# Kernel optimization log

Measured on AMD Instinct MI355X. Metric: run time of the kernel, lower is better.

Reference implementation:

```python
import jax, jax.numpy as jnp
import numpy as np

B, N, E = 128, 400, 512      # batch, spatial locations, encoder_size
SH, H, A = 256, 512, 256     # structural_hidden, cell_content_hidden, attention_size
EMB, V, T = 256, 1000, 256   # embedding_size, vocabulary_size, num_timesteps
START = 0                    # token2integer['<start>']


def setup_inputs() -> dict:
    key = jax.random.key(0)
    ks = jax.random.split(key, 16)
    s = lambda k, shape, scale=0.05: jax.random.normal(k, shape, jnp.float32) * scale
    return {
        'encoded_features_map': jax.random.normal(ks[0], (B, N, E), jnp.float32),
        'structural_hidden_state': jax.random.normal(ks[1], (1, B, SH), jnp.float32),
        'cell_content_target': jax.random.randint(ks[2], (B, T), 0, V),
        # attention params (linear projections + score vector)
        'Wf': s(ks[3], (E, A)), 'bf': jnp.zeros((A,), jnp.float32),
        'Ws': s(ks[4], (SH, A)), 'bs': jnp.zeros((A,), jnp.float32),
        'Wc': s(ks[5], (H, A)), 'bc': jnp.zeros((A,), jnp.float32),
        'v_att': s(ks[6], (A,)),
        # embedding table
        'emb_table': s(ks[7], (V, EMB), 0.02),
        # GRU params (torch layout: [3H, in] / [3H, H], gate order r,z,n)
        'W_ih': s(ks[8], (3 * H, E + EMB)), 'W_hh': s(ks[9], (3 * H, H)),
        'b_ih': jnp.zeros((3 * H,), jnp.float32), 'b_hh': jnp.zeros((3 * H,), jnp.float32),
        # output projection
        'W_fc': s(ks[10], (H, V)), 'b_fc': jnp.zeros((V,), jnp.float32),
    }


def _decode(encoded_features_map, structural_hidden_state, cell_content_target,
            Wf, bf, Ws, bs, Wc, bc, v_att, emb_table, W_ih, W_hh, b_ih, b_hh, W_fc, b_fc):
    # precompute static attention projections
    feat_proj = jnp.einsum('bne,ea->bna', encoded_features_map, Wf) + bf   # [B,N,A]
    struct_proj = structural_hidden_state[0] @ Ws + bs                      # [B,A]

    def step(carry, tok_next):
        h, tok = carry                                  # h: [B,H], tok: [B]
        # additive attention over spatial locations
        att = jnp.tanh(feat_proj + (struct_proj + h @ Wc + bc)[:, None, :])  # [B,N,A]
        alpha = jax.nn.softmax(att @ v_att, axis=-1)                          # [B,N]
        context = jnp.einsum('bn,bne->be', alpha, encoded_features_map)      # [B,E]
        # embed previous token, concat, single GRU step
        x = jnp.concatenate([context, emb_table[tok]], axis=1)               # [B,E+EMB]
        gi = x @ W_ih.T + b_ih                                               # [B,3H]
        gh = h @ W_hh.T + b_hh                                               # [B,3H]
        r = jax.nn.sigmoid(gi[:, :H] + gh[:, :H])
        z = jax.nn.sigmoid(gi[:, H:2 * H] + gh[:, H:2 * H])
        n = jnp.tanh(gi[:, 2 * H:] + r * gh[:, 2 * H:])
        h_new = (1.0 - z) * n + z * h
        logits = h_new @ W_fc + b_fc                                         # [B,V]
        # per-step CrossEntropyLoss (mean over batch), teacher forcing
        logp = jax.nn.log_softmax(logits, axis=-1)
        loss_t = -jnp.mean(jnp.take_along_axis(logp, tok_next[:, None], axis=1))
        return (h_new, tok_next), (logits, loss_t)

    h0 = jnp.zeros((encoded_features_map.shape[0], H), jnp.float32)
    tok0 = jnp.full((encoded_features_map.shape[0],), START, cell_content_target.dtype)
    tgt_t = cell_content_target.T                                            # [T,B]
    _, (predictions, losses) = jax.lax.scan(step, (h0, tok0), tgt_t)
    nT = tgt_t.shape[0]
    bsz = encoded_features_map.shape[0]
    loss = losses.sum() / nT / bsz
    return predictions, loss


def reference(encoded_features_map, structural_hidden_state, cell_content_target,
              Wf, bf, Ws, bs, Wc, bc, v_att, emb_table, W_ih, W_hh, b_ih, b_hh, W_fc, b_fc):
    return _decode(encoded_features_map, structural_hidden_state, cell_content_target,
                   Wf, bf, Ws, bs, Wc, bc, v_att, emb_table, W_ih, W_hh, b_ih, b_hh, W_fc, b_fc)
```

## Files before the change

kernel.cpp:

```cpp
#include <hip/hip_runtime.h>
#include <math.h>

#define BB  128
#define NN  400
#define EE  512
#define SHD 256
#define HH  512
#define AA  256
#define EMBD 256
#define VV  1000
#define TT  256
#define TH3 (3*HH)
#define BNROWS (BB*NN)
#define PRED_STRIDE (BB*VV)
#define NPRED ((size_t)TT*BB*VV)

__device__ __forceinline__ float tanh_fast(float x){
    float e = __expf(2.f*x);
    return 1.f - 2.f*__builtin_amdgcn_rcpf(e + 1.f);
}


__global__ void k_zero(float* __restrict__ hbuf0, float* __restrict__ loss_acc){
    int i = blockIdx.x*blockDim.x + threadIdx.x;
    if (i < BB*HH) hbuf0[i] = 0.f;
    if (i == 0) loss_acc[0] = 0.f;
}

__global__ __launch_bounds__(256) void k_featproj(
    const float* __restrict__ feats, const float* __restrict__ Wf,
    const float* __restrict__ bf, float* __restrict__ fp)
{
    __shared__ float As[32][65];
    __shared__ float Bs[32][65];
    int row0 = blockIdx.x*64, col0 = blockIdx.y*64;
    int tx = threadIdx.x & 15, ty = threadIdx.x >> 4;
    float acc[4][4] = {};
    for (int k0 = 0; k0 < EE; k0 += 32){
        for (int idx = threadIdx.x; idx < 64*32; idx += 256){
            int r = idx >> 5, kk = idx & 31;
            As[kk][r] = feats[(size_t)(row0 + r)*EE + k0 + kk];
        }
        for (int idx = threadIdx.x; idx < 32*64; idx += 256){
            int kk = idx >> 6, c = idx & 63;
            Bs[kk][c] = Wf[(size_t)(k0 + kk)*AA + col0 + c];
        }
        __syncthreads();
        #pragma unroll
        for (int kk = 0; kk < 32; ++kk){
            float a0 = As[kk][ty*4+0], a1 = As[kk][ty*4+1], a2 = As[kk][ty*4+2], a3 = As[kk][ty*4+3];
            float b0 = Bs[kk][tx*4+0], b1 = Bs[kk][tx*4+1], b2 = Bs[kk][tx*4+2], b3 = Bs[kk][tx*4+3];
            acc[0][0] += a0*b0; acc[0][1] += a0*b1; acc[0][2] += a0*b2; acc[0][3] += a0*b3;
            acc[1][0] += a1*b0; acc[1][1] += a1*b1; acc[1][2] += a1*b2; acc[1][3] += a1*b3;
            acc[2][0] += a2*b0; acc[2][1] += a2*b1; acc[2][2] += a2*b2; acc[2][3] += a2*b3;
            acc[3][0] += a3*b0; acc[3][1] += a3*b1; acc[3][2] += a3*b2; acc[3][3] += a3*b3;
        }
        __syncthreads();
    }
    #pragma unroll
    for (int i = 0; i < 4; ++i){
        #pragma unroll
        for (int j = 0; j < 4; ++j){
            int col = col0 + tx*4 + j;
            fp[(size_t)(row0 + ty*4 + i)*AA + col] = acc[i][j] + bf[col];
        }
    }
}

__global__ void k_wembT(const float* __restrict__ Wih, float* __restrict__ wT){
    int i = blockIdx.x*blockDim.x + threadIdx.x;
    if (i >= EMBD*TH3) return;
    int m = i / TH3, r = i - m*TH3;
    wT[i] = Wih[(size_t)r*(EE+EMBD) + EE + m];
}

__global__ __launch_bounds__(256) void k_embproj(
    const float* __restrict__ emb, const float* __restrict__ wT,
    const float* __restrict__ bih, float* __restrict__ ep)
{
    __shared__ float el[16][257];
    int vt = blockIdx.x, rc = blockIdx.y;
    for (int idx = threadIdx.x; idx < 16*EMBD; idx += 256){
        int v = idx >> 8, m = idx & 255;
        int gv = vt*16 + v;
        el[v][m] = (gv < VV) ? emb[(size_t)gv*EMBD + m] : 0.f;
    }
    __syncthreads();
    int r = rc*256 + threadIdx.x;
    float acc[16] = {};
    for (int m = 0; m < EMBD; ++m){
        float w = wT[(size_t)m*TH3 + r];
        #pragma unroll
        for (int v = 0; v < 16; ++v) acc[v] += el[v][m]*w;
    }
    float bb_ = bih[r];
    #pragma unroll
    for (int v = 0; v < 16; ++v){
        int gv = vt*16 + v;
        if (gv < VV) ep[(size_t)gv*TH3 + r] = acc[v] + bb_;
    }
}

__global__ void k_structproj(const float* __restrict__ sh, const float* __restrict__ Ws,
                             const float* __restrict__ bs, float* __restrict__ sp){
    __shared__ float sl[SHD];
    int b = blockIdx.x;
    for (int i = threadIdx.x; i < SHD; i += 256) sl[i] = sh[(size_t)b*SHD + i];
    __syncthreads();
    int a = threadIdx.x;
    float acc = 0.f;
    for (int s = 0; s < SHD; ++s) acc += sl[s]*Ws[(size_t)s*AA + a];
    sp[(size_t)b*AA + a] = acc + bs[a];
}


__device__ __forceinline__ void logits_body(int tpred, int bt, int vt,
    const float* __restrict__ hsrc, const float* __restrict__ Wfc,
    const float* __restrict__ bfc, float* __restrict__ preds, float* hl)
{
    for (int idx = threadIdx.x; idx < 8*HH; idx += 512){
        int bl = idx >> 9;
        hl[idx] = hsrc[(size_t)(bt*8+bl)*HH + (idx & 511)];
    }
    __syncthreads();
    for (int o = threadIdx.x; o < 1000; o += 512){
        int bl = o / 125, vl = o - bl*125;
        int v = vt*125 + vl;
        const float* wcol = Wfc + v;
        const float* hrow = hl + bl*HH;
        float acc = 0.f;
        #pragma unroll 4
        for (int h = 0; h < HH; ++h) acc += hrow[h]*wcol[(size_t)h*VV];
        __builtin_nontemporal_store(acc + bfc[v],
            &preds[(size_t)tpred*PRED_STRIDE + (size_t)(bt*8+bl)*VV + v]);
    }
}

__device__ __forceinline__ void loss_body(int tpred, int lb,
    const float* __restrict__ preds, const int* __restrict__ tgt, float* loss_acc)
{
    int w = threadIdx.x >> 6, lane = threadIdx.x & 63;
    float contrib = 0.f;
    for (int rr = 0; rr < 2; ++rr){
        int row = lb*16 + w*2 + rr;
        const float* p = preds + (size_t)tpred*PRED_STRIDE + (size_t)row*VV;
        float m = -1e30f;
        for (int i = lane; i < VV; i += 64) m = fmaxf(m, __builtin_nontemporal_load(p + i));
        #pragma unroll
        for (int off = 32; off; off >>= 1) m = fmaxf(m, __shfl_xor(m, off));
        float s = 0.f;
        for (int i = lane; i < VV; i += 64) s += expf(__builtin_nontemporal_load(p + i) - m);
        #pragma unroll
        for (int off = 32; off; off >>= 1) s += __shfl_xor(s, off);
        if (lane == 0) contrib += m + logf(s) - p[tgt[(size_t)row*TT + tpred]];
    }
    if (lane == 0) atomicAdd(loss_acc, contrib);
}

__global__ __launch_bounds__(512) void k_attn(int t,
    const float* __restrict__ fp, const float* __restrict__ feats,
    const float* __restrict__ sp, const float* __restrict__ bc,
    const float* __restrict__ vatt, const float* __restrict__ qpart,
    const float* __restrict__ hin, const float* __restrict__ Wfc,
    const float* __restrict__ bfc,
    float* __restrict__ pctx, float* __restrict__ psum, float* __restrict__ preds)
{
    __shared__ __align__(16) float smem[AA + 8*EE + 8];
    if (blockIdx.x >= 256){
        if (t == 0) return;
        int lb = blockIdx.x - 256;
        logits_body(t-1, lb >> 3, lb & 7, hin, Wfc, bfc, preds, smem);
        return;
    }
    int b = blockIdx.x >> 1, half = blockIdx.x & 1;
    float* qs = smem;
    float* px = smem + AA;
    float* ps = smem + AA + 8*EE;
    if (threadIdx.x < AA){
        int a = threadIdx.x;
        float val = sp[(size_t)b*AA + a] + bc[a];
        if (t > 0){
            #pragma unroll 4
            for (int jt = 0; jt < 32; ++jt) val += qpart[((size_t)jt*BB + b)*AA + a];
        }
        qs[a] = val;
    }
    __syncthreads();
    int w = threadIdx.x >> 6, lane = threadIdx.x & 63;
    float4 v4 = ((const float4*)vatt)[lane];
    float4 q4 = ((const float4*)qs)[lane];
    float acc0=0,acc1=0,acc2=0,acc3=0,acc4=0,acc5=0,acc6=0,acc7=0;
    float psum_r = 0.f;
    const int nbase = half*200;
    for (int k = 0; k < 25; ++k){
        int n = nbase + w + 8*k;
        const float4* fr4 = (const float4*)(fp + ((size_t)b*NN + n)*AA);
        float4 xv = fr4[lane];
        float s = v4.x*tanh_fast(xv.x+q4.x) + v4.y*tanh_fast(xv.y+q4.y)
                + v4.z*tanh_fast(xv.z+q4.z) + v4.w*tanh_fast(xv.w+q4.w);
        #pragma unroll
        for (int off = 32; off; off >>= 1) s += __shfl_xor(s, off);
        float e = __expf(s);
        psum_r += e;
        const float4* f4 = (const float4*)(feats + ((size_t)b*NN + n)*EE) + lane*2;
        float4 fa = f4[0], fb = f4[1];
        acc0 += e*fa.x; acc1 += e*fa.y; acc2 += e*fa.z; acc3 += e*fa.w;
        acc4 += e*fb.x; acc5 += e*fb.y; acc6 += e*fb.z; acc7 += e*fb.w;
    }
    float* myrow = px + w*EE + lane*8;
    myrow[0]=acc0; myrow[1]=acc1; myrow[2]=acc2; myrow[3]=acc3;
    myrow[4]=acc4; myrow[5]=acc5; myrow[6]=acc6; myrow[7]=acc7;
    if (lane == 0) ps[w] = psum_r;
    __syncthreads();
    for (int e = threadIdx.x; e < EE; e += 512){
        float tot = 0.f;
        #pragma unroll
        for (int ww = 0; ww < 8; ++ww) tot += px[ww*EE + e];
        pctx[((size_t)b*2 + half)*EE + e] = tot;
    }
    if (threadIdx.x == 0){
        float tot = 0.f;
        #pragma unroll
        for (int ww = 0; ww < 8; ++ww) tot += ps[ww];
        psum[b*2 + half] = tot;
    }
}

__global__ __launch_bounds__(512) void k_gru(int t,
    const float* __restrict__ pctx, const float* __restrict__ psum,
    const float* __restrict__ hin, float* __restrict__ hout,
    const float* __restrict__ Wih, const float* __restrict__ Whh,
    const float* __restrict__ bhh, const float* __restrict__ embp,
    const int* __restrict__ tgt, const float* __restrict__ Wc,
    float* __restrict__ qpart, const float* __restrict__ preds,
    float* __restrict__ loss_acc)
{
    if (blockIdx.x >= 256){
        if (t == 0) return;
        loss_body(t-1, (int)blockIdx.x - 256, preds, tgt, loss_acc);
        return;
    }
    __shared__ __align__(16) float stage[16][516];
    __shared__ float part[2][16][16][3];
    __shared__ float gi_s[16][16][3];
    __shared__ float hn_l[16][16];
    __shared__ float inv_l[16];
    int bt = blockIdx.x >> 5, jt = blockIdx.x & 31;
    int bg = bt*16, jbase = jt*16;
    int p = threadIdx.x & 255, role = threadIdx.x >> 8;
    int b = p & 15, j = p >> 4, r0 = jbase + j;
    if (threadIdx.x < 16){
        int bb_ = threadIdx.x;
        inv_l[bb_] = 1.f/(psum[(bg+bb_)*2] + psum[(bg+bb_)*2+1]);
    }
    __syncthreads();
    for (int idx = threadIdx.x; idx < 16*EE; idx += 512){
        int bb_ = idx >> 9, e = idx & 511;
        stage[bb_][e] = (pctx[((size_t)(bg+bb_)*2)*EE + e] +
                         pctx[((size_t)(bg+bb_)*2+1)*EE + e]) * inv_l[bb_];
    }
    __syncthreads();
    {
        const float* w0 = Wih + (size_t)r0*(EE+EMBD);
        const float* w1 = w0 + (size_t)512*(EE+EMBD);
        const float* w2 = w0 + (size_t)1024*(EE+EMBD);
        float ar=0, az=0, an=0;
        int e0 = role*256;
        const float4* srow = (const float4*)&stage[b][0];
        #pragma unroll 4
        for (int e4 = e0/4; e4 < e0/4 + 64; ++e4){
            float4 c = srow[e4];
            int e = e4*4;
            ar += c.x*w0[e] + c.y*w0[e+1] + c.z*w0[e+2] + c.w*w0[e+3];
            az += c.x*w1[e] + c.y*w1[e+1] + c.z*w1[e+2] + c.w*w1[e+3];
            an += c.x*w2[e] + c.y*w2[e+1] + c.z*w2[e+2] + c.w*w2[e+3];
        }
        part[role][b][j][0] = ar; part[role][b][j][1] = az; part[role][b][j][2] = an;
    }
    __syncthreads();
    if (threadIdx.x < 256){
        int tok = (t == 0) ? 0 : tgt[(size_t)(bg+b)*TT + (t-1)];
        const float* er = embp + (size_t)tok*TH3 + r0;
        gi_s[b][j][0] = part[0][b][j][0] + part[1][b][j][0] + er[0];
        gi_s[b][j][1] = part[0][b][j][1] + part[1][b][j][1] + er[512];
        gi_s[b][j][2] = part[0][b][j][2] + part[1][b][j][2] + er[1024];
    }
    __syncthreads();
    for (int idx = threadIdx.x; idx < 16*HH; idx += 512){
        int bb_ = idx >> 9, e = idx & 511;
        stage[bb_][e] = hin[(size_t)(bg+bb_)*HH + e];
    }
    __syncthreads();
    {
        const float* w0 = Whh + (size_t)r0*HH;
        const float* w1 = w0 + (size_t)512*HH;
        const float* w2 = w0 + (size_t)1024*HH;
        float ar=0, az=0, an=0;
        int e0 = role*256;
        const float4* srow = (const float4*)&stage[b][0];
        #pragma unroll 4
        for (int e4 = e0/4; e4 < e0/4 + 64; ++e4){
            float4 c = srow[e4];
            int e = e4*4;
            ar += c.x*w0[e] + c.y*w0[e+1] + c.z*w0[e+2] + c.w*w0[e+3];
            az += c.x*w1[e] + c.y*w1[e+1] + c.z*w1[e+2] + c.w*w1[e+3];
            an += c.x*w2[e] + c.y*w2[e+1] + c.z*w2[e+2] + c.w*w2[e+3];
        }
        part[role][b][j][0] = ar; part[role][b][j][1] = az; part[role][b][j][2] = an;
    }
    __syncthreads();
    if (threadIdx.x < 256){
        float ghr = part[0][b][j][0] + part[1][b][j][0] + bhh[r0];
        float ghz = part[0][b][j][1] + part[1][b][j][1] + bhh[r0+512];
        float ghn = part[0][b][j][2] + part[1][b][j][2] + bhh[r0+1024];
        float rr = 1.f/(1.f + expf(-(gi_s[b][j][0] + ghr)));
        float zz = 1.f/(1.f + expf(-(gi_s[b][j][1] + ghz)));
        float nn = tanhf(gi_s[b][j][2] + rr*ghn);
        float hval = stage[b][r0];
        float hn = (1.f - zz)*nn + zz*hval;
        hout[(size_t)(bg+b)*HH + r0] = hn;
        hn_l[b][j] = hn;
    }
    __syncthreads();
    for (int o = threadIdx.x; o < 16*AA; o += 512){
        int bb_ = o >> 8, a = o & 255;
        float acc = 0.f;
        #pragma unroll
        for (int jj = 0; jj < 16; ++jj) acc += hn_l[bb_][jj]*Wc[(size_t)(jbase+jj)*AA + a];
        qpart[((size_t)jt*BB + bg + bb_)*AA + a] = acc;
    }
}

__global__ __launch_bounds__(512) void k_logits_ep(int tpred, const float* __restrict__ hsrc,
    const float* __restrict__ Wfc, const float* __restrict__ bfc, float* __restrict__ preds)
{
    __shared__ __align__(16) float hl[8*HH];
    logits_body(tpred, (int)blockIdx.x >> 3, (int)blockIdx.x & 7, hsrc, Wfc, bfc, preds, hl);
}

__global__ __launch_bounds__(512) void k_loss_ep(int tpred, const float* __restrict__ preds,
    const int* __restrict__ tgt, float* __restrict__ loss_acc)
{
    loss_body(tpred, (int)blockIdx.x, preds, tgt, loss_acc);
}

__global__ void k_final(const float* __restrict__ loss_acc, float* __restrict__ out){
    out[0] = loss_acc[0] * (1.f/4194304.f);
}

extern "C" void kernel_launch(void* const* d_in, const int* in_sizes, int n_in,
                              void* d_out, int out_size, void* d_ws, size_t ws_size,
                              hipStream_t stream)
{
    const float* feats = (const float*)d_in[0];
    const float* shs   = (const float*)d_in[1];
    const int*   tgt   = (const int*)d_in[2];
    const float* Wf    = (const float*)d_in[3];
    const float* bf    = (const float*)d_in[4];
    const float* Ws    = (const float*)d_in[5];
    const float* bs    = (const float*)d_in[6];
    const float* Wc    = (const float*)d_in[7];
    const float* bc    = (const float*)d_in[8];
    const float* vatt  = (const float*)d_in[9];
    const float* emb   = (const float*)d_in[10];
    const float* Wih   = (const float*)d_in[11];
    const float* Whh   = (const float*)d_in[12];
    const float* bih   = (const float*)d_in[13];
    const float* bhh   = (const float*)d_in[14];
    const float* Wfc   = (const float*)d_in[15];
    const float* bfc   = (const float*)d_in[16];
    float* preds = (float*)d_out;

    char* base = (char*)d_ws;
    size_t off = 0;
    auto alloc = [&](size_t nfloats) -> float* {
        float* ptr = (float*)(base + off);
        off += ((nfloats*sizeof(float) + 255)/256)*256;
        return ptr;
    };
    float* fp    = alloc((size_t)BNROWS*AA);
    float* embp  = alloc((size_t)VV*TH3);
    float* wT    = alloc((size_t)EMBD*TH3);
    float* sp    = alloc((size_t)BB*AA);
    float* qpart = alloc((size_t)32*BB*AA);
    float* pctx  = alloc((size_t)BB*2*EE);
    float* psum  = alloc((size_t)BB*2);
    float* hbuf  = alloc((size_t)2*BB*HH);
    float* lacc  = alloc(16);
    (void)ws_size; (void)in_sizes; (void)n_in; (void)out_size;

    k_zero<<<(BB*HH + 511)/512, 512, 0, stream>>>(hbuf, lacc);
    k_featproj<<<dim3(BNROWS/64, AA/64), 256, 0, stream>>>(feats, Wf, bf, fp);
    k_wembT<<<(EMBD*TH3)/256, 256, 0, stream>>>(Wih, wT);
    k_embproj<<<dim3(63, TH3/256), 256, 0, stream>>>(emb, wT, bih, embp);
    k_structproj<<<BB, 256, 0, stream>>>(shs, Ws, bs, sp);

    for (int t = 0; t < TT; ++t){
        const float* hin = hbuf + (size_t)(t & 1)*BB*HH;
        float*       hout = hbuf + (size_t)((t + 1) & 1)*BB*HH;
        k_attn<<<384, 512, 0, stream>>>(t, fp, feats, sp, bc, vatt, qpart,
                                        hin, Wfc, bfc, pctx, psum, preds);
        k_gru<<<264, 512, 0, stream>>>(t, pctx, psum, hin, hout, Wih, Whh, bhh,
                                       embp, tgt, Wc, qpart, preds, lacc);
    }
    k_logits_ep<<<128, 512, 0, stream>>>(TT-1, hbuf, Wfc, bfc, preds);
    k_loss_ep<<<8, 512, 0, stream>>>(TT-1, preds, tgt, lacc);
    k_final<<<1, 1, 0, stream>>>(lacc, preds + NPRED);
}
```

Baseline: 30.90 ms.

## Transpose feature projection and FC weights, split attention into quarters, merge GRU matvecs

The feature projection is stored transposed ([B,A,N]) so attention threads each own one spatial position and read coalesced along N, and the work per batch is split across four blocks instead of two. The output FC weights are pre-transposed so the logits loop reads each vocabulary row contiguously with float4 loads. The GRU input and hidden matvecs are merged into a single pass with both operands staged in shared memory, which removes extra barriers, and the bc bias is folded into the struct projection. The trade-offs are more workspace memory, an extra transpose kernel at setup, and more partial sums to combine in the GRU stage.

New measurement: 32.84 ms. 1.06x slower.

```diff
diff --git a/kernel.cpp b/kernel.cpp
--- a/kernel.cpp
+++ b/kernel.cpp
@@ -29,7 +29,7 @@
 
 __global__ __launch_bounds__(256) void k_featproj(
     const float* __restrict__ feats, const float* __restrict__ Wf,
-    const float* __restrict__ bf, float* __restrict__ fp)
+    const float* __restrict__ bf, float* __restrict__ fpT)
 {
     __shared__ float As[32][65];
     __shared__ float Bs[32][65];
@@ -59,10 +59,12 @@
     }
     #pragma unroll
     for (int i = 0; i < 4; ++i){
+        int row = row0 + ty*4 + i;
+        int b = row/NN, n = row - b*NN;
         #pragma unroll
         for (int j = 0; j < 4; ++j){
             int col = col0 + tx*4 + j;
-            fp[(size_t)(row0 + ty*4 + i)*AA + col] = acc[i][j] + bf[col];
+            fpT[((size_t)b*AA + col)*NN + n] = acc[i][j] + bf[col];
         }
     }
 }
@@ -72,6 +74,13 @@
     if (i >= EMBD*TH3) return;
     int m = i / TH3, r = i - m*TH3;
     wT[i] = Wih[(size_t)r*(EE+EMBD) + EE + m];
+}
+
+__global__ void k_wfcT(const float* __restrict__ Wfc, float* __restrict__ WfcT){
+    int i = blockIdx.x*blockDim.x + threadIdx.x;
+    if (i >= VV*HH) return;
+    int v = i / HH, h = i - v*HH;
+    WfcT[i] = Wfc[(size_t)h*VV + v];
 }
 
 __global__ __launch_bounds__(256) void k_embproj(
@@ -102,7 +111,8 @@
 }
 
 __global__ void k_structproj(const float* __restrict__ sh, const float* __restrict__ Ws,
-                             const float* __restrict__ bs, float* __restrict__ sp){
+                             const float* __restrict__ bs, const float* __restrict__ bc,
+                             float* __restrict__ sp){
     __shared__ float sl[SHD];
     int b = blockIdx.x;
     for (int i = threadIdx.x; i < SHD; i += 256) sl[i] = sh[(size_t)b*SHD + i];
@@ -110,12 +120,12 @@
     int a = threadIdx.x;
     float acc = 0.f;
     for (int s = 0; s < SHD; ++s) acc += sl[s]*Ws[(size_t)s*AA + a];
-    sp[(size_t)b*AA + a] = acc + bs[a];
+    sp[(size_t)b*AA + a] = acc + bs[a] + bc[a];
 }
 
 
 __device__ __forceinline__ void logits_body(int tpred, int bt, int vt,
-    const float* __restrict__ hsrc, const float* __restrict__ Wfc,
+    const float* __restrict__ hsrc, const float* __restrict__ WfcT,
     const float* __restrict__ bfc, float* __restrict__ preds, float* hl)
 {
     for (int idx = threadIdx.x; idx < 8*HH; idx += 512){
@@ -126,11 +136,14 @@
     for (int o = threadIdx.x; o < 1000; o += 512){
         int bl = o / 125, vl = o - bl*125;
         int v = vt*125 + vl;
-        const float* wcol = Wfc + v;
-        const float* hrow = hl + bl*HH;
+        const float4* wrow = (const float4*)(WfcT + (size_t)v*HH);
+        const float4* hrow = (const float4*)(hl + bl*HH);
         float acc = 0.f;
-        #pragma unroll 4
-        for (int h = 0; h < HH; ++h) acc += hrow[h]*wcol[(size_t)h*VV];
+        #pragma unroll 8
+        for (int h4 = 0; h4 < HH/4; ++h4){
+            float4 w = wrow[h4], hh = hrow[h4];
+            acc += w.x*hh.x + w.y*hh.y + w.z*hh.z + w.w*hh.w;
+        }
         __builtin_nontemporal_store(acc + bfc[v],
             &preds[(size_t)tpred*PRED_STRIDE + (size_t)(bt*8+bl)*VV + v]);
     }
@@ -140,9 +153,10 @@
     const float* __restrict__ preds, const int* __restrict__ tgt, float* loss_acc)
 {
     int w = threadIdx.x >> 6, lane = threadIdx.x & 63;
+    int nw = blockDim.x >> 6;
     float contrib = 0.f;
-    for (int rr = 0; rr < 2; ++rr){
-        int row = lb*16 + w*2 + rr;
+    for (int ri = w; ri < 16; ri += nw){
+        int row = lb*16 + ri;
         const float* p = preds + (size_t)tpred*PRED_STRIDE + (size_t)row*VV;
         float m = -1e30f;
         for (int i = lane; i < VV; i += 64) m = fmaxf(m, __builtin_nontemporal_load(p + i));
@@ -158,71 +172,71 @@
 }
 
 __global__ __launch_bounds__(512) void k_attn(int t,
-    const float* __restrict__ fp, const float* __restrict__ feats,
-    const float* __restrict__ sp, const float* __restrict__ bc,
-    const float* __restrict__ vatt, const float* __restrict__ qpart,
-    const float* __restrict__ hin, const float* __restrict__ Wfc,
-    const float* __restrict__ bfc,
+    const float* __restrict__ fpT, const float* __restrict__ feats,
+    const float* __restrict__ sp2, const float* __restrict__ vatt,
+    const float* __restrict__ qpart, const float* __restrict__ hin,
+    const float* __restrict__ WfcT, const float* __restrict__ bfc,
     float* __restrict__ pctx, float* __restrict__ psum, float* __restrict__ preds)
 {
-    __shared__ __align__(16) float smem[AA + 8*EE + 8];
-    if (blockIdx.x >= 256){
+    __shared__ __align__(16) float smem[4160];
+    if (blockIdx.x >= 512){
         if (t == 0) return;
-        int lb = blockIdx.x - 256;
-        logits_body(t-1, lb >> 3, lb & 7, hin, Wfc, bfc, preds, smem);
+        int lb = blockIdx.x - 512;
+        logits_body(t-1, lb >> 3, lb & 7, hin, WfcT, bfc, preds, smem);
         return;
     }
-    int b = blockIdx.x >> 1, half = blockIdx.x & 1;
+    int b = blockIdx.x >> 2, qtr = blockIdx.x & 3;
+    const int nbase = qtr*100;
     float* qs = smem;
-    float* px = smem + AA;
-    float* ps = smem + AA + 8*EE;
+    float* vs = smem + 256;
+    float* sA = smem + 512;
+    float* al = smem + 1024;
     if (threadIdx.x < AA){
         int a = threadIdx.x;
-        float val = sp[(size_t)b*AA + a] + bc[a];
+        float val = sp2[(size_t)b*AA + a];
         if (t > 0){
             #pragma unroll 4
             for (int jt = 0; jt < 32; ++jt) val += qpart[((size_t)jt*BB + b)*AA + a];
         }
         qs[a] = val;
-    }
-    __syncthreads();
-    int w = threadIdx.x >> 6, lane = threadIdx.x & 63;
-    float4 v4 = ((const float4*)vatt)[lane];
-    float4 q4 = ((const float4*)qs)[lane];
-    float acc0=0,acc1=0,acc2=0,acc3=0,acc4=0,acc5=0,acc6=0,acc7=0;
-    float psum_r = 0.f;
-    const int nbase = half*200;
-    for (int k = 0; k < 25; ++k){
-        int n = nbase + w + 8*k;
-        const float4* fr4 = (const float4*)(fp + ((size_t)b*NN + n)*AA);
-        float4 xv = fr4[lane];
-        float s = v4.x*tanh_fast(xv.x+q4.x) + v4.y*tanh_fast(xv.y+q4.y)
-                + v4.z*tanh_fast(xv.z+q4.z) + v4.w*tanh_fast(xv.w+q4.w);
-        #pragma unroll
-        for (int off = 32; off; off >>= 1) s += __shfl_xor(s, off);
-        float e = __expf(s);
-        psum_r += e;
-        const float4* f4 = (const float4*)(feats + ((size_t)b*NN + n)*EE) + lane*2;
-        float4 fa = f4[0], fb = f4[1];
-        acc0 += e*fa.x; acc1 += e*fa.y; acc2 += e*fa.z; acc3 += e*fa.w;
-        acc4 += e*fb.x; acc5 += e*fb.y; acc6 += e*fb.z; acc7 += e*fb.w;
-    }
-    float* myrow = px + w*EE + lane*8;
-    myrow[0]=acc0; myrow[1]=acc1; myrow[2]=acc2; myrow[3]=acc3;
-    myrow[4]=acc4; myrow[5]=acc5; myrow[6]=acc6; myrow[7]=acc7;
-    if (lane == 0) ps[w] = psum_r;
-    __syncthreads();
-    for (int e = threadIdx.x; e < EE; e += 512){
-        float tot = 0.f;
-        #pragma unroll
-        for (int ww = 0; ww < 8; ++ww) tot += px[ww*EE + e];
-        pctx[((size_t)b*2 + half)*EE + e] = tot;
-    }
-    if (threadIdx.x == 0){
-        float tot = 0.f;
-        #pragma unroll
-        for (int ww = 0; ww < 8; ++ww) tot += ps[ww];
-        psum[b*2 + half] = tot;
+        vs[a] = vatt[a];
+    }
+    __syncthreads();
+    int nl = threadIdx.x & 127, ah = threadIdx.x >> 7;
+    float sacc = 0.f;
+    if (nl < 100){
+        const float* fr = fpT + ((size_t)b*AA + ah*64)*NN + nbase + nl;
+        #pragma unroll 4
+        for (int i = 0; i < 64; ++i)
+            sacc += vs[ah*64 + i]*tanh_fast(fr[(size_t)i*NN] + qs[ah*64 + i]);
+    }
+    sA[ah*128 + nl] = sacc;
+    __syncthreads();
+    if (threadIdx.x < 128){
+        float e = 0.f;
+        if (threadIdx.x < 100)
+            e = __expf(sA[threadIdx.x] + sA[128 + threadIdx.x] +
+                       sA[256 + threadIdx.x] + sA[384 + threadIdx.x]);
+        al[threadIdx.x] = e;
+    }
+    __syncthreads();
+    if (threadIdx.x < 64){
+        float e = al[threadIdx.x] + al[threadIdx.x + 64];
+        #pragma unroll
+        for (int off = 32; off; off >>= 1) e += __shfl_xor(e, off);
+        if (threadIdx.x == 0) psum[b*4 + qtr] = e;
+    }
+    {
+        int e = threadIdx.x;
+        float c0=0.f, c1=0.f, c2=0.f, c3=0.f;
+        const float* fb = feats + ((size_t)b*NN + nbase)*EE + e;
+        for (int n = 0; n < 100; n += 4){
+            c0 += al[n+0]*fb[(size_t)(n+0)*EE];
+            c1 += al[n+1]*fb[(size_t)(n+1)*EE];
+            c2 += al[n+2]*fb[(size_t)(n+2)*EE];
+            c3 += al[n+3]*fb[(size_t)(n+3)*EE];
+        }
+        pctx[((size_t)b*4 + qtr)*EE + e] = (c0+c1)+(c2+c3);
     }
 }
 
@@ -236,88 +250,71 @@
     float* __restrict__ loss_acc)
 {
     if (blockIdx.x >= 256){
-        if (t == 0) return;
-        loss_body(t-1, (int)blockIdx.x - 256, preds, tgt, loss_acc);
+        if (t > 0) loss_body(t-1, (int)blockIdx.x - 256, preds, tgt, loss_acc);
         return;
     }
-    __shared__ __align__(16) float stage[16][516];
-    __shared__ float part[2][16][16][3];
-    __shared__ float gi_s[16][16][3];
+    __shared__ __align__(16) float stC[16][516];
+    __shared__ __align__(16) float stH[16][516];
+    __shared__ float pGI[2][16][16][3];
+    __shared__ float pGH[2][16][16][3];
     __shared__ float hn_l[16][16];
-    __shared__ float inv_l[16];
     int bt = blockIdx.x >> 5, jt = blockIdx.x & 31;
     int bg = bt*16, jbase = jt*16;
     int p = threadIdx.x & 255, role = threadIdx.x >> 8;
     int b = p & 15, j = p >> 4, r0 = jbase + j;
-    if (threadIdx.x < 16){
-        int bb_ = threadIdx.x;
-        inv_l[bb_] = 1.f/(psum[(bg+bb_)*2] + psum[(bg+bb_)*2+1]);
-    }
-    __syncthreads();
+    for (int idx = threadIdx.x; idx < 16*HH; idx += 512){
+        int bb_ = idx >> 9, e = idx & 511;
+        stH[bb_][e] = hin[(size_t)(bg+bb_)*HH + e];
+    }
     for (int idx = threadIdx.x; idx < 16*EE; idx += 512){
         int bb_ = idx >> 9, e = idx & 511;
-        stage[bb_][e] = (pctx[((size_t)(bg+bb_)*2)*EE + e] +
-                         pctx[((size_t)(bg+bb_)*2+1)*EE + e]) * inv_l[bb_];
+        const float* ps4 = psum + (size_t)(bg+bb_)*4;
+        float iv = 1.f/(ps4[0]+ps4[1]+ps4[2]+ps4[3]);
+        const float* pc = pctx + (size_t)(bg+bb_)*4*EE + e;
+        stC[bb_][e] = (pc[0] + pc[EE] + pc[2*(size_t)EE] + pc[3*(size_t)EE]) * iv;
     }
     __syncthreads();
     {
-        const float* w0 = Wih + (size_t)r0*(EE+EMBD);
-        const float* w1 = w0 + (size_t)512*(EE+EMBD);
-        const float* w2 = w0 + (size_t)1024*(EE+EMBD);
-        float ar=0, az=0, an=0;
-        int e0 = role*256;
-        const float4* srow = (const float4*)&stage[b][0];
+        const float4* w0 = (const float4*)(Wih + (size_t)r0*(EE+EMBD));
+        const float4* w1 = (const float4*)(Wih + (size_t)(r0+512)*(EE+EMBD));
+        const float4* w2 = (const float4*)(Wih + (size_t)(r0+1024)*(EE+EMBD));
+        const float4* u0 = (const float4*)(Whh + (size_t)r0*HH);
+        const float4* u1 = (const float4*)(Whh + (size_t)(r0+512)*HH);
+        const float4* u2 = (const float4*)(Whh + (size_t)(r0+1024)*HH);
+        float ar=0,az=0,an=0, br=0,bz=0,bn=0;
+        const float4* crow = (const float4*)&stC[b][0];
+        const float4* hrow = (const float4*)&stH[b][0];
+        int e40 = role*64;
         #pragma unroll 4
-        for (int e4 = e0/4; e4 < e0/4 + 64; ++e4){
-            float4 c = srow[e4];
-            int e = e4*4;
-            ar += c.x*w0[e] + c.y*w0[e+1] + c.z*w0[e+2] + c.w*w0[e+3];
-            az += c.x*w1[e] + c.y*w1[e+1] + c.z*w1[e+2] + c.w*w1[e+3];
-            an += c.x*w2[e] + c.y*w2[e+1] + c.z*w2[e+2] + c.w*w2[e+3];
-        }
-        part[role][b][j][0] = ar; part[role][b][j][1] = az; part[role][b][j][2] = an;
+        for (int e4 = e40; e4 < e40 + 64; ++e4){
+            float4 c = crow[e4]; float4 h = hrow[e4];
+            float4 a0 = w0[e4], a1 = w1[e4], a2 = w2[e4];
+            float4 b0 = u0[e4], b1 = u1[e4], b2 = u2[e4];
+            ar += c.x*a0.x + c.y*a0.y + c.z*a0.z + c.w*a0.w;
+            az += c.x*a1.x + c.y*a1.y + c.z*a1.z + c.w*a1.w;
+            an += c.x*a2.x + c.y*a2.y + c.z*a2.z + c.w*a2.w;
+            br += h.x*b0.x + h.y*b0.y + h.z*b0.z + h.w*b0.w;
+            bz += h.x*b1.x + h.y*b1.y + h.z*b1.z + h.w*b1.w;
+            bn += h.x*b2.x + h.y*b2.y + h.z*b2.z + h.w*b2.w;
+        }
+        pGI[role][b][j][0]=ar; pGI[role][b][j][1]=az; pGI[role][b][j][2]=an;
+        pGH[role][b][j][0]=br; pGH[role][b][j][1]=bz; pGH[role][b][j][2]=bn;
     }
     __syncthreads();
     if (threadIdx.x < 256){
         int tok = (t == 0) ? 0 : tgt[(size_t)(bg+b)*TT + (t-1)];
         const float* er = embp + (size_t)tok*TH3 + r0;
-        gi_s[b][j][0] = part[0][b][j][0] + part[1][b][j][0] + er[0];
-        gi_s[b][j][1] = part[0][b][j][1] + part[1][b][j][1] + er[512];
-        gi_s[b][j][2] = part[0][b][j][2] + part[1][b][j][2] + er[1024];
-    }
-    __syncthreads();
-    for (int idx = threadIdx.x; idx < 16*HH; idx += 512){
-        int bb_ = idx >> 9, e = idx & 511;
-        stage[bb_][e] = hin[(size_t)(bg+bb_)*HH + e];
-    }
-    __syncthreads();
-    {
-        const float* w0 = Whh + (size_t)r0*HH;
-        const float* w1 = w0 + (size_t)512*HH;
-        const float* w2 = w0 + (size_t)1024*HH;
-        float ar=0, az=0, an=0;
-        int e0 = role*256;
-        const float4* srow = (const float4*)&stage[b][0];
-        #pragma unroll 4
-        for (int e4 = e0/4; e4 < e0/4 + 64; ++e4){
-            float4 c = srow[e4];
-            int e = e4*4;
-            ar += c.x*w0[e] + c.y*w0[e+1] + c.z*w0[e+2] + c.w*w0[e+3];
-            az += c.x*w1[e] + c.y*w1[e+1] + c.z*w1[e+2] + c.w*w1[e+3];
-            an += c.x*w2[e] + c.y*w2[e+1] + c.z*w2[e+2] + c.w*w2[e+3];
-        }
-        part[role][b][j][0] = ar; part[role][b][j][1] = az; part[role][b][j][2] = an;
-    }
-    __syncthreads();
-    if (threadIdx.x < 256){
-        float ghr = part[0][b][j][0] + part[1][b][j][0] + bhh[r0];
-        float ghz = part[0][b][j][1] + part[1][b][j][1] + bhh[r0+512];
-        float ghn = part[0][b][j][2] + part[1][b][j][2] + bhh[r0+1024];
-        float rr = 1.f/(1.f + expf(-(gi_s[b][j][0] + ghr)));
-        float zz = 1.f/(1.f + expf(-(gi_s[b][j][1] + ghz)));
-        float nn = tanhf(gi_s[b][j][2] + rr*ghn);
-        float hval = stage[b][r0];
-        float hn = (1.f - zz)*nn + zz*hval;
+        float gir = pGI[0][b][j][0]+pGI[1][b][j][0] + er[0];
+        float giz = pGI[0][b][j][1]+pGI[1][b][j][1] + er[512];
+        float gin = pGI[0][b][j][2]+pGI[1][b][j][2] + er[1024];
+        float ghr = pGH[0][b][j][0]+pGH[1][b][j][0] + bhh[r0];
+        float ghz = pGH[0][b][j][1]+pGH[1][b][j][1] + bhh[r0+512];
+        float ghn = pGH[0][b][j][2]+pGH[1][b][j][2] + bhh[r0+1024];
+        float rr = 1.f/(1.f + expf(-(gir + ghr)));
+        float zz = 1.f/(1.f + expf(-(giz + ghz)));
+        float nn2 = tanhf(gin + rr*ghn);
+        float hv = stH[b][r0];
+        float hn = (1.f - zz)*nn2 + zz*hv;
         hout[(size_t)(bg+b)*HH + r0] = hn;
         hn_l[b][j] = hn;
     }
@@ -332,10 +329,10 @@
 }
 
 __global__ __launch_bounds__(512) void k_logits_ep(int tpred, const float* __restrict__ hsrc,
-    const float* __restrict__ Wfc, const float* __restrict__ bfc, float* __restrict__ preds)
+    const float* __restrict__ WfcT, const float* __restrict__ bfc, float* __restrict__ preds)
 {
     __shared__ __align__(16) float hl[8*HH];
-    logits_body(tpred, (int)blockIdx.x >> 3, (int)blockIdx.x & 7, hsrc, Wfc, bfc, preds, hl);
+    logits_body(tpred, (int)blockIdx.x >> 3, (int)blockIdx.x & 7, hsrc, WfcT, bfc, preds, hl);
 }
 
 __global__ __launch_bounds__(512) void k_loss_ep(int tpred, const float* __restrict__ preds,
@@ -378,32 +375,34 @@
         off += ((nfloats*sizeof(float) + 255)/256)*256;
         return ptr;
     };
-    float* fp    = alloc((size_t)BNROWS*AA);
+    float* fpT   = alloc((size_t)BNROWS*AA);
     float* embp  = alloc((size_t)VV*TH3);
     float* wT    = alloc((size_t)EMBD*TH3);
-    float* sp    = alloc((size_t)BB*AA);
+    float* wfcT  = alloc((size_t)VV*HH);
+    float* sp2   = alloc((size_t)BB*AA);
     float* qpart = alloc((size_t)32*BB*AA);
-    float* pctx  = alloc((size_t)BB*2*EE);
-    float* psum  = alloc((size_t)BB*2);
+    float* pctx  = alloc((size_t)BB*4*EE);
+    float* psum  = alloc((size_t)BB*4);
     float* hbuf  = alloc((size_t)2*BB*HH);
     float* lacc  = alloc(16);
     (void)ws_size; (void)in_sizes; (void)n_in; (void)out_size;
 
     k_zero<<<(BB*HH + 511)/512, 512, 0, stream>>>(hbuf, lacc);
-    k_featproj<<<dim3(BNROWS/64, AA/64), 256, 0, stream>>>(feats, Wf, bf, fp);
+    k_featproj<<<dim3(BNROWS/64, AA/64), 256, 0, stream>>>(feats, Wf, bf, fpT);
     k_wembT<<<(EMBD*TH3)/256, 256, 0, stream>>>(Wih, wT);
+    k_wfcT<<<(VV*HH + 255)/256, 256, 0, stream>>>(Wfc, wfcT);
     k_embproj<<<dim3(63, TH3/256), 256, 0, stream>>>(emb, wT, bih, embp);
-    k_structproj<<<BB, 256, 0, stream>>>(shs, Ws, bs, sp);
+    k_structproj<<<BB, 256, 0, stream>>>(shs, Ws, bs, bc, sp2);
 
     for (int t = 0; t < TT; ++t){
         const float* hin = hbuf + (size_t)(t & 1)*BB*HH;
         float*       hout = hbuf + (size_t)((t + 1) & 1)*BB*HH;
-        k_attn<<<384, 512, 0, stream>>>(t, fp, feats, sp, bc, vatt, qpart,
-                                        hin, Wfc, bfc, pctx, psum, preds);
+        k_attn<<<640, 512, 0, stream>>>(t, fpT, feats, sp2, vatt, qpart,
+                                        hin, wfcT, bfc, pctx, psum, preds);
         k_gru<<<264, 512, 0, stream>>>(t, pctx, psum, hin, hout, Wih, Whh, bhh,
                                        embp, tgt, Wc, qpart, preds, lacc);
     }
-    k_logits_ep<<<128, 512, 0, stream>>>(TT-1, hbuf, Wfc, bfc, preds);
+    k_logits_ep<<<128, 512, 0, stream>>>(TT-1, hbuf, wfcT, bfc, preds);
     k_loss_ep<<<8, 512, 0, stream>>>(TT-1, preds, tgt, lacc);
     k_final<<<1, 1, 0, stream>>>(lacc, preds + NPRED);
 }
```
